# Kernel tuning notes

Measured on AMD Instinct MI355X. Metric: run time of the kernel, lower is better.

## Reference

```python
import jax, jax.numpy as jnp
import numpy as np
from jax import lax

BN_EPS = 1e-5
LRELU_SLOPE = 0.01  # nn.LeakyReLU default negative_slope


def setup_inputs() -> dict:
    key = jax.random.key(0)
    k1, k2, k3, k4 = jax.random.split(key, 4)
    N, Cin, Cout, K, P = 500000, 32, 32, 27, 250000
    features = jax.random.normal(k1, (N, Cin), dtype=jnp.float32)
    weight = jax.random.normal(k2, (K, Cin, Cout), dtype=jnp.float32) * 0.05
    gamma = jnp.ones((Cout,), dtype=jnp.float32)
    beta = jnp.zeros((Cout,), dtype=jnp.float32)
    pairs_in = jax.random.randint(k3, (K, P), 0, N, dtype=jnp.int32)
    pairs_out = jax.random.randint(k4, (K, P), 0, N, dtype=jnp.int32)
    return {"features": features, "weight": weight, "gamma": gamma,
            "beta": beta, "pairs_in": pairs_in, "pairs_out": pairs_out}


def _subm_conv(features, weight, pairs_in, pairs_out):
    # Submanifold sparse conv: for each kernel offset k, gather input rows,
    # multiply by W[k], scatter-add into output rows. N_out == N_in.
    N = features.shape[0]
    Cout = weight.shape[-1]
    out0 = jnp.zeros((N, Cout), dtype=features.dtype)

    def step(acc, xs):
        w_k, pi_k, po_k = xs                  # [Cin,Cout], [P], [P]
        gathered = features[pi_k]             # [P, Cin] gather
        contrib = gathered @ w_k              # [P, Cout]
        return acc.at[po_k].add(contrib), None  # scatter-add

    out, _ = lax.scan(step, out0, (weight, pairs_in, pairs_out))
    return out


def reference(features, weight, gamma, beta, pairs_in, pairs_out):
    conv = _subm_conv(features, weight, pairs_in, pairs_out)   # [N, Cout]
    # Original forward: features = norm(act(features)) -> LeakyReLU THEN BN
    act = jnp.where(conv >= 0, conv, LRELU_SLOPE * conv)
    mean = jnp.mean(act, axis=0)
    var = jnp.var(act, axis=0)                # BatchNorm1d training stats over N
    y = (act - mean) * lax.rsqrt(var + BN_EPS) * gamma + beta
    return y
```

## Files before the change

### kernel.cpp

```cpp
#include <hip/hip_runtime.h>
#include <hip/hip_fp16.h>

#define CIN 32
#define COUT 32
#define LRELU_SLOPE 0.01f
#define BN_EPS 1e-5f
#define CHUNK 2048
#define KMAX 27

typedef _Float16 half2_t __attribute__((ext_vector_type(2)));

#if __has_builtin(__builtin_amdgcn_fdot2)
#define FDOT2(a, b, c) __builtin_amdgcn_fdot2((a), (b), (c), false)
#else
static __device__ __forceinline__ float fdot2_sw(half2_t a, half2_t b, float c) {
    return (float)a.x * (float)b.x + (float)a.y * (float)b.y + c;
}
#define FDOT2(a, b, c) fdot2_sw((a), (b), (c))
#endif

#if __has_builtin(__builtin_amdgcn_cvt_pkrtz)
#define CVTPK(x, y) __builtin_bit_cast(half2_t, __builtin_amdgcn_cvt_pkrtz((x), (y)))
#else
static __device__ __forceinline__ half2_t cvtpk_sw(float x, float y) {
    half2_t r; r.x = (_Float16)x; r.y = (_Float16)y; return r;
}
#define CVTPK(x, y) cvtpk_sw((x), (y))
#endif

union HU { uint4 u; half2_t h[4]; };
union FU { uint4 u; float f[4]; };


__global__ void __launch_bounds__(256) hist_kernel(
    const int* __restrict__ po, int* __restrict__ cnt, int E)
{
    int i0 = (blockIdx.x * blockDim.x + threadIdx.x) * 4;
    if (i0 + 3 < E) {
        int4 v = *(const int4*)(po + i0);
        atomicAdd(&cnt[v.x], 1);
        atomicAdd(&cnt[v.y], 1);
        atomicAdd(&cnt[v.z], 1);
        atomicAdd(&cnt[v.w], 1);
    } else {
        for (int i = i0; i < E; ++i) atomicAdd(&cnt[po[i]], 1);
    }
}

__global__ void __launch_bounds__(256) blocksum_kernel(
    const int* __restrict__ cnt, int* __restrict__ bsum, int N)
{
    int base = blockIdx.x * CHUNK + threadIdx.x * 8;
    int s = 0;
#pragma unroll
    for (int j = 0; j < 8; ++j) { int i = base + j; if (i < N) s += cnt[i]; }
#pragma unroll
    for (int off = 1; off < 64; off <<= 1) s += __shfl_xor(s, off);
    __shared__ int wsum[4];
    if ((threadIdx.x & 63) == 0) wsum[threadIdx.x >> 6] = s;
    __syncthreads();
    if (threadIdx.x == 0) bsum[blockIdx.x] = wsum[0] + wsum[1] + wsum[2] + wsum[3];
}

__global__ void __launch_bounds__(256) scanblk_kernel(
    const int* __restrict__ bsum, int* __restrict__ boffs, int nb)
{
    __shared__ int ts[256];
    int tid = threadIdx.x;
    int v[4]; int s = 0;
#pragma unroll
    for (int j = 0; j < 4; ++j) {
        int i = tid * 4 + j;
        v[j] = (i < nb) ? bsum[i] : 0;
        s += v[j];
    }
    ts[tid] = s;
    __syncthreads();
    for (int off = 1; off < 256; off <<= 1) {
        int add = (tid >= off) ? ts[tid - off] : 0;
        __syncthreads();
        ts[tid] += add;
        __syncthreads();
    }
    int run = ts[tid] - s;
#pragma unroll
    for (int j = 0; j < 4; ++j) {
        int i = tid * 4 + j;
        if (i < nb) { boffs[i] = run; run += v[j]; }
    }
}

__global__ void __launch_bounds__(256) scatteroffs_kernel(
    int* __restrict__ cnt, int* __restrict__ cursors,
    const int* __restrict__ boffs, int N)
{
    int tid = threadIdx.x;
    int lane = tid & 63;
    int wv = tid >> 6;
    int base = blockIdx.x * CHUNK + tid * 8;
    int c[8]; int tsum = 0;
#pragma unroll
    for (int j = 0; j < 8; ++j) { int i = base + j; c[j] = (i < N) ? cnt[i] : 0; tsum += c[j]; }
    int x = tsum;
#pragma unroll
    for (int off = 1; off < 64; off <<= 1) {
        int y = __shfl_up(x, off);
        if (lane >= off) x += y;
    }
    __shared__ int wtot[4];
    if (lane == 63) wtot[wv] = x;
    __syncthreads();
    int woff = boffs[blockIdx.x];
    for (int w = 0; w < wv; ++w) woff += wtot[w];
    int off = woff + x - tsum;
#pragma unroll
    for (int j = 0; j < 8; ++j) {
        int i = base + j;
        if (i < N) { cnt[i] = off; cursors[i] = off; off += c[j]; }
    }
}

__global__ void __launch_bounds__(256) scatter_kernel(
    const int* __restrict__ pairs_out, const int* __restrict__ pairs_in,
    int* __restrict__ cursors, int* __restrict__ sorted, int P)
{
    int p0 = (blockIdx.x * blockDim.x + threadIdx.x) * 4;
    int k = blockIdx.y;
    const int* po = pairs_out + (size_t)k * P;
    const int* pi = pairs_in + (size_t)k * P;
    if (p0 + 3 < P) {
        int4 o4 = *(const int4*)(po + p0);
        int4 i4 = *(const int4*)(pi + p0);
        int s0 = atomicAdd(&cursors[o4.x], 1); sorted[s0] = (i4.x << 6) | k;
        int s1 = atomicAdd(&cursors[o4.y], 1); sorted[s1] = (i4.y << 6) | k;
        int s2 = atomicAdd(&cursors[o4.z], 1); sorted[s2] = (i4.z << 6) | k;
        int s3 = atomicAdd(&cursors[o4.w], 1); sorted[s3] = (i4.w << 6) | k;
    } else {
        for (int p = p0; p < P; ++p) {
            int slot = atomicAdd(&cursors[po[p]], 1);
            sorted[slot] = (pi[p] << 6) | k;
        }
    }
}


__global__ void __launch_bounds__(256) cvt_kernel(
    const float* __restrict__ f, __half* __restrict__ o, int n8)
{
    int i = blockIdx.x * 256 + threadIdx.x;
    if (i >= n8) return;
    const float4* s = (const float4*)f + (size_t)i * 2;
    float4 a = s[0], b = s[1];
    union { uint4 u; __half h[8]; } r;
    r.h[0] = __float2half(a.x); r.h[1] = __float2half(a.y);
    r.h[2] = __float2half(a.z); r.h[3] = __float2half(a.w);
    r.h[4] = __float2half(b.x); r.h[5] = __float2half(b.y);
    r.h[6] = __float2half(b.z); r.h[7] = __float2half(b.w);
    ((uint4*)o)[i] = r.u;
}


template<int PC>
__global__ void __launch_bounds__(512, 8) fused_wave_kernel(
    const float* __restrict__ features,
    const __half* __restrict__ feat16,
    const float* __restrict__ weight,
    const int* __restrict__ sorted,
    const int* __restrict__ offsets,
    float* __restrict__ out,
    float* __restrict__ gstats,
    int N, int E, int rowBase, int rowCount, int rpw, int KW)
{
    __shared__ __align__(16) __half wlds[KMAX * 512];
    __shared__ float sred[8][16];
    __shared__ float qred[8][16];

    const int co_base = ((blockIdx.x >> 3) & 1) << 4;
    const int rg = (blockIdx.x & 7) | ((blockIdx.x >> 4) << 3);

    for (int s = threadIdx.x; s < KW * 512; s += 512) {
        int co_l = s & 15, c = (s >> 4) & 31, k = s >> 9;
        wlds[k * 512 + co_l * 32 + c] =
            __float2half(weight[k * 1024 + c * 32 + co_base + co_l]);
    }
    __syncthreads();

    const int lane = threadIdx.x & 63;
    const int wv = threadIdx.x >> 6;
    const int j = lane & 3;
    const int co_l = lane >> 2;
    const int gw = rg * 8 + wv;
    const int wlane_off = lane << 4;
    const char* wbase = (const char*)wlds;
    const char* fbase = PC ? (const char*)feat16 : (const char*)features;

    float ssum = 0.f, qsum = 0.f;

    int i0 = rowBase + gw * rpw;
    int i1 = i0 + rpw;
    int rend = rowBase + rowCount; if (rend > N) rend = N;
    if (i1 > rend) i1 = rend;

#define LOADE(F0, F1, W0, IDX) do {                                               \
    int _ii = (IDX); _ii = _ii < 63 ? _ii : 63;                                   \
    int _pk = __builtin_amdgcn_readlane(pkl, _ii);                                \
    W0 = *(const uint4*)(wbase + ((_pk & 63) << 10) + wlane_off);                 \
    if (PC) {                                                                     \
        const char* _sb = fbase + (unsigned)(_pk & 0xFFFFFFC0);                   \
        F0 = *(const uint4*)(_sb + (j << 4));                                     \
    } else {                                                                      \
        const char* _sb = fbase + ((size_t)(unsigned)(_pk & 0xFFFFFFC0) << 1);    \
        F0 = *(const uint4*)(_sb + (j << 5));                                     \
        F1 = *(const uint4*)(_sb + (j << 5) + 16);                                \
    }                                                                             \
} while (0)

#define DOTS(F0, F1, W0) do {                                                     \
    HU _w; _w.u = W0;                                                             \
    half2_t _p0, _p1, _p2, _p3;                                                   \
    if (PC) {                                                                     \
        HU _f; _f.u = F0;                                                         \
        _p0 = _f.h[0]; _p1 = _f.h[1]; _p2 = _f.h[2]; _p3 = _f.h[3];               \
    } else {                                                                      \
        FU _a, _b; _a.u = F0; _b.u = F1;                                          \
        _p0 = CVTPK(_a.f[0], _a.f[1]); _p1 = CVTPK(_a.f[2], _a.f[3]);             \
        _p2 = CVTPK(_b.f[0], _b.f[1]); _p3 = CVTPK(_b.f[2], _b.f[3]);             \
    }                                                                             \
    acc0 = FDOT2(_p0, _w.h[0], acc0); acc1 = FDOT2(_p1, _w.h[1], acc1);           \
    acc0 = FDOT2(_p2, _w.h[2], acc0); acc1 = FDOT2(_p3, _w.h[3], acc1);           \
} while (0)

#define WINDOW() do {                                                             \
    uint4 fA0, fA1, wA0, fB0, fB1, wB0, fC0, fC1, wC0, fD0, fD1, wD0;             \
    LOADE(fA0, fA1, wA0, 0);                                                      \
    LOADE(fB0, fB1, wB0, 1);                                                      \
    LOADE(fC0, fC1, wC0, 2);                                                      \
    LOADE(fD0, fD1, wD0, 3);                                                      \
    for (int e = 0; e < m; e += 4) {                                              \
        DOTS(fA0, fA1, wA0); LOADE(fA0, fA1, wA0, e + 4);                         \
        if (e + 1 < m) { DOTS(fB0, fB1, wB0); LOADE(fB0, fB1, wB0, e + 5); }      \
        if (e + 2 < m) { DOTS(fC0, fC1, wC0); LOADE(fC0, fC1, wC0, e + 6); }      \
        if (e + 3 < m) { DOTS(fD0, fD1, wD0); LOADE(fD0, fD1, wD0, e + 7); }      \
    }                                                                             \
} while (0)

    if (i0 < rend) {
        int beg = offsets[i0];
        int pklA;
        {
            int end0 = (i0 == N - 1) ? E : offsets[i0 + 1];
            int m0 = end0 - beg; if (m0 > 64) m0 = 64;
            pklA = (lane < m0) ? sorted[beg + lane] : 0;
        }
        for (int r = i0; r < i1; ++r) {
            int end = (r == N - 1) ? E : offsets[r + 1];
            int pklB = 0;
            if (r + 1 < i1) {
                int endn = (r + 1 == N - 1) ? E : offsets[r + 2];
                int mn = endn - end; if (mn > 64) mn = 64;
                pklB = (lane < mn) ? sorted[end + lane] : 0;
            }
            float acc0 = 0.f, acc1 = 0.f;
            if (end > beg) {
                {
                    int m = end - beg; if (m > 64) m = 64;
                    int pkl = pklA;
                    WINDOW();
                }
                for (int base = beg + 64; base < end; base += 64) {
                    int m = end - base; if (m > 64) m = 64;
                    int pkl = (lane < m) ? sorted[base + lane] : 0;
                    WINDOW();
                }
            }
            float acc = acc0 + acc1;
            acc += __shfl_xor(acc, 1);
            acc += __shfl_xor(acc, 2);
            float act = acc >= 0.f ? acc : LRELU_SLOPE * acc;
            if (j == 0) out[(size_t)r * COUT + co_base + co_l] = act;
            ssum += act; qsum += act * act;
            beg = end; pklA = pklB;
        }
    }

#undef WINDOW
#undef LOADE
#undef DOTS

    sred[wv][co_l] = ssum;
    qred[wv][co_l] = qsum;
    __syncthreads();
    if (threadIdx.x < 16) {
        int t = threadIdx.x;
        float S = 0.f, Q = 0.f;
#pragma unroll
        for (int w = 0; w < 8; ++w) { S += sred[w][t]; Q += qred[w][t]; }
        atomicAdd(&gstats[co_base + t], S);
        atomicAdd(&gstats[32 + co_base + t], Q);
    }
}

__global__ void __launch_bounds__(256) norm2_kernel(
    float* __restrict__ data, const float* __restrict__ stats,
    const float* __restrict__ gamma, const float* __restrict__ beta,
    int n4, float invN)
{
    int i = blockIdx.x * blockDim.x + threadIdx.x;
    if (i >= n4) return;
    int qd = i & 7;
    float sc[4], bs[4];
#pragma unroll
    for (int j = 0; j < 4; ++j) {
        int c = qd * 4 + j;
        float m = stats[c] * invN;
        float v = stats[32 + c] * invN - m * m;
        float inv = rsqrtf(v + BN_EPS);
        sc[j] = inv * gamma[c];
        bs[j] = beta[c] - m * sc[j];
    }
    float4* d4 = (float4*)data;
    float4 a = d4[i];
    float4 y;
    y.x = a.x * sc[0] + bs[0];
    y.y = a.y * sc[1] + bs[1];
    y.z = a.z * sc[2] + bs[2];
    y.w = a.w * sc[3] + bs[3];
    d4[i] = y;
}


__global__ void __launch_bounds__(256) conv_atomic_kernel(
    const float* __restrict__ features,
    const float* __restrict__ weight,
    const int* __restrict__ pairs_in,
    const int* __restrict__ pairs_out,
    float* __restrict__ out,
    int P)
{
    int p = blockIdx.x * blockDim.x + threadIdx.x;
    int k = blockIdx.y;
    if (p >= P) return;
    int pi = pairs_in[(size_t)k * P + p];
    int po = pairs_out[(size_t)k * P + p];
    const float4* __restrict__ frow = (const float4*)(features + (size_t)pi * CIN);
    const float* __restrict__ wk = weight + (size_t)k * CIN * COUT;
    float acc[COUT];
#pragma unroll
    for (int co = 0; co < COUT; ++co) acc[co] = 0.f;
#pragma unroll
    for (int c4 = 0; c4 < CIN / 4; ++c4) {
        float4 f = frow[c4];
        float fv[4] = {f.x, f.y, f.z, f.w};
#pragma unroll
        for (int j = 0; j < 4; ++j) {
            const float* __restrict__ wr = wk + (c4 * 4 + j) * COUT;
#pragma unroll
            for (int co = 0; co < COUT; ++co)
                acc[co] = fmaf(fv[j], wr[co], acc[co]);
        }
    }
    float* orow = out + (size_t)po * COUT;
#pragma unroll
    for (int co = 0; co < COUT; ++co)
        atomicAdd(orow + co, acc[co]);
}

__device__ __forceinline__ float4 lrelu4(float4 v) {
    float4 a;
    a.x = v.x >= 0.f ? v.x : LRELU_SLOPE * v.x;
    a.y = v.y >= 0.f ? v.y : LRELU_SLOPE * v.y;
    a.z = v.z >= 0.f ? v.z : LRELU_SLOPE * v.z;
    a.w = v.w >= 0.f ? v.w : LRELU_SLOPE * v.w;
    return a;
}

__global__ void __launch_bounds__(256) stats_fb_kernel(
    const float* __restrict__ conv, float* __restrict__ stats, int n4)
{
    const float4* __restrict__ c4p = (const float4*)conv;
    int stride = blockDim.x * gridDim.x;
    float4 s = {0.f, 0.f, 0.f, 0.f};
    float4 q = {0.f, 0.f, 0.f, 0.f};
    for (int i = blockIdx.x * blockDim.x + threadIdx.x; i < n4; i += stride) {
        float4 a = lrelu4(c4p[i]);
        s.x += a.x; s.y += a.y; s.z += a.z; s.w += a.w;
        q.x += a.x * a.x; q.y += a.y * a.y; q.z += a.z * a.z; q.w += a.w * a.w;
    }
#pragma unroll
    for (int off = 8; off < 64; off <<= 1) {
        s.x += __shfl_xor(s.x, off); s.y += __shfl_xor(s.y, off);
        s.z += __shfl_xor(s.z, off); s.w += __shfl_xor(s.w, off);
        q.x += __shfl_xor(q.x, off); q.y += __shfl_xor(q.y, off);
        q.z += __shfl_xor(q.z, off); q.w += __shfl_xor(q.w, off);
    }
    __shared__ float4 rs[4][8];
    __shared__ float4 rq[4][8];
    int lane = threadIdx.x & 63;
    int w = threadIdx.x >> 6;
    if (lane < 8) { rs[w][lane] = s; rq[w][lane] = q; }
    __syncthreads();
    if (threadIdx.x < 8) {
        int qd = threadIdx.x;
        float4 S = {0.f, 0.f, 0.f, 0.f};
        float4 Q = {0.f, 0.f, 0.f, 0.f};
        for (int ww = 0; ww < 4; ++ww) {
            float4 a = rs[ww][qd], b = rq[ww][qd];
            S.x += a.x; S.y += a.y; S.z += a.z; S.w += a.w;
            Q.x += b.x; Q.y += b.y; Q.z += b.z; Q.w += b.w;
        }
        atomicAdd(&stats[qd * 4 + 0], S.x); atomicAdd(&stats[qd * 4 + 1], S.y);
        atomicAdd(&stats[qd * 4 + 2], S.z); atomicAdd(&stats[qd * 4 + 3], S.w);
        atomicAdd(&stats[32 + qd * 4 + 0], Q.x); atomicAdd(&stats[32 + qd * 4 + 1], Q.y);
        atomicAdd(&stats[32 + qd * 4 + 2], Q.z); atomicAdd(&stats[32 + qd * 4 + 3], Q.w);
    }
}

__global__ void __launch_bounds__(256) norm_fb_kernel(
    float* __restrict__ data, const float* __restrict__ stats,
    const float* __restrict__ gamma, const float* __restrict__ beta,
    int n4, float invN)
{
    int i = blockIdx.x * blockDim.x + threadIdx.x;
    if (i >= n4) return;
    int qd = i & 7;
    float sc[4], bs[4];
#pragma unroll
    for (int j = 0; j < 4; ++j) {
        int c = qd * 4 + j;
        float m = stats[c] * invN;
        float v = stats[32 + c] * invN - m * m;
        float inv = rsqrtf(v + BN_EPS);
        sc[j] = inv * gamma[c];
        bs[j] = beta[c] - m * sc[j];
    }
    float4* d4 = (float4*)data;
    float4 a = lrelu4(d4[i]);
    float4 y;
    y.x = a.x * sc[0] + bs[0];
    y.y = a.y * sc[1] + bs[1];
    y.z = a.z * sc[2] + bs[2];
    y.w = a.w * sc[3] + bs[3];
    d4[i] = y;
}

extern "C" void kernel_launch(void* const* d_in, const int* in_sizes, int n_in,
                              void* d_out, int out_size, void* d_ws, size_t ws_size,
                              hipStream_t stream) {
    const float* features = (const float*)d_in[0];
    const float* weight   = (const float*)d_in[1];
    const float* gamma    = (const float*)d_in[2];
    const float* beta     = (const float*)d_in[3];
    const int* pairs_in   = (const int*)d_in[4];
    const int* pairs_out  = (const int*)d_in[5];
    float* out = (float*)d_out;

    int N  = in_sizes[0] / CIN;
    int KW = in_sizes[1] / (CIN * COUT);
    int P  = in_sizes[4] / KW;
    int E  = KW * P;
    int n4 = N * (COUT / 4);

    char* wsb = (char*)d_ws;
    float* stats  = (float*)wsb;
    int* offsets  = (int*)(wsb + 256);
    int* cursors  = offsets + N;
    int* bsum     = cursors + N;
    int* boffs    = bsum + 1024;
    int* sorted   = boffs + 1024;
    __half* feat16 = (__half*)(((uintptr_t)(sorted + E) + 15) & ~(uintptr_t)15);

    size_t need1 = 256 + ((size_t)2 * N + 2048 + E) * 4;
    size_t need2 = need1 + 16 + (size_t)N * CIN * 2;

    bool fast = (ws_size >= need1) && (KW <= KMAX) && (N <= (1 << 24));
    bool preconv = fast && (ws_size >= need2);

    if (fast) {
        hipMemsetAsync(stats, 0, 256, stream);
        hipMemsetAsync(offsets, 0, (size_t)N * sizeof(int), stream);

        hist_kernel<<<(E / 4 + 255) / 256, 256, 0, stream>>>(pairs_out, offsets, E);

        int nb = (N + CHUNK - 1) / CHUNK;
        blocksum_kernel<<<nb, 256, 0, stream>>>(offsets, bsum, N);
        scanblk_kernel<<<1, 256, 0, stream>>>(bsum, boffs, nb);
        scatteroffs_kernel<<<nb, 256, 0, stream>>>(offsets, cursors, boffs, N);

        dim3 sgrid((P + 1023) / 1024, KW);
        scatter_kernel<<<sgrid, 256, 0, stream>>>(pairs_out, pairs_in, cursors, sorted, P);

        const int NRG = 512;
        int totW = NRG * 8;
        int rows0 = (N + 1) / 2;
        int rows1 = N - rows0;
        int rpw0 = (rows0 + totW - 1) / totW;
        int rpw1 = (rows1 + totW - 1) / totW;

        if (preconv) {
            cvt_kernel<<<(N * (CIN / 8) + 255) / 256, 256, 0, stream>>>(
                features, feat16, N * (CIN / 8));
            fused_wave_kernel<1><<<NRG * 2, 512, 0, stream>>>(
                features, feat16, weight, sorted, offsets, out, stats,
                N, E, 0, rows0, rpw0, KW);
            fused_wave_kernel<1><<<NRG * 2, 512, 0, stream>>>(
                features, feat16, weight, sorted, offsets, out, stats,
                N, E, rows0, rows1, rpw1, KW);
        } else {
            fused_wave_kernel<0><<<NRG * 2, 512, 0, stream>>>(
                features, feat16, weight, sorted, offsets, out, stats,
                N, E, 0, rows0, rpw0, KW);
            fused_wave_kernel<0><<<NRG * 2, 512, 0, stream>>>(
                features, feat16, weight, sorted, offsets, out, stats,
                N, E, rows0, rows1, rpw1, KW);
        }

        norm2_kernel<<<(n4 + 255) / 256, 256, 0, stream>>>(out, stats, gamma, beta,
                                                           n4, 1.0f / (float)N);
    } else {
        hipMemsetAsync(d_out, 0, (size_t)out_size * sizeof(float), stream);
        hipMemsetAsync(d_ws, 0, 64 * sizeof(float), stream);
        dim3 cgrid((P + 255) / 256, KW);
        conv_atomic_kernel<<<cgrid, 256, 0, stream>>>(features, weight, pairs_in,
                                                      pairs_out, (float*)d_out, P);
        stats_fb_kernel<<<512, 256, 0, stream>>>((const float*)d_out, (float*)d_ws, n4);
        norm_fb_kernel<<<(n4 + 255) / 256, 256, 0, stream>>>((float*)d_out, (float*)d_ws,
                                                             gamma, beta, n4,
                                                             1.0f / (float)N);
    }
}
```

Before: 1.442 ms.

## Sort pairs in two phases via coarse bucket binning before atomic scatter

Replaces the single random-scatter counting-sort pass with a two-phase approach: pairs are first binned into 256 coarse buckets of output rows using shared-memory local histograms and staging, then a resolve pass does the per-row atomic scatter. Because binned entries are grouped by output range, the per-row cursor atomics and sorted writes in the resolve pass become more localized and cache-friendly. In exchange it adds an extra E*8-byte intermediate buffer, an extra read/write pass over all pairs, and two more kernel launches. It only runs when the workspace is large enough.

```diff
diff --git a/kernel.cpp b/kernel.cpp
--- a/kernel.cpp
+++ b/kernel.cpp
@@ -7,6 +7,8 @@
 #define BN_EPS 1e-5f
 #define CHUNK 2048
 #define KMAX 27
+#define NBUCK 256
+#define BCH 4096
 
 typedef _Float16 half2_t __attribute__((ext_vector_type(2)));
 
@@ -117,6 +119,114 @@
     for (int j = 0; j < 8; ++j) {
         int i = base + j;
         if (i < N) { cnt[i] = off; cursors[i] = off; off += c[j]; }
+    }
+}
+
+
+__global__ void __launch_bounds__(256) bucketinit_kernel(
+    const int* __restrict__ offsets, int* __restrict__ bucketCur,
+    int N, int E, int shift)
+{
+    int b = threadIdx.x;
+    long idx = (long)b << shift;
+    bucketCur[b] = (idx < N) ? offsets[idx] : E;
+}
+
+__global__ void __launch_bounds__(256) bin_kernel(
+    const int* __restrict__ pairs_out, const int* __restrict__ pairs_in,
+    int* __restrict__ bucketCur, uint2* __restrict__ binned,
+    int P, int shift)
+{
+    __shared__ uint2 buf[BCH];
+    __shared__ int hist[NBUCK];
+    __shared__ int ts[NBUCK];
+    __shared__ int lbase[NBUCK];
+    __shared__ int gbase[NBUCK];
+    __shared__ int lcur[NBUCK];
+    int tid = threadIdx.x;
+    int k = blockIdx.y;
+    int p0 = blockIdx.x * BCH;
+    const int* po = pairs_out + (size_t)k * P;
+    const int* pi = pairs_in  + (size_t)k * P;
+
+    hist[tid] = 0;
+    __syncthreads();
+
+    int myP[16], myV[16];
+#pragma unroll
+    for (int j = 0; j < 4; ++j) {
+        int idx = p0 + j * 1024 + tid * 4;
+        if (idx + 3 < P) {
+            int4 o4 = *(const int4*)(po + idx);
+            int4 i4 = *(const int4*)(pi + idx);
+            myP[j*4+0] = o4.x; myV[j*4+0] = (i4.x << 6) | k;
+            myP[j*4+1] = o4.y; myV[j*4+1] = (i4.y << 6) | k;
+            myP[j*4+2] = o4.z; myV[j*4+2] = (i4.z << 6) | k;
+            myP[j*4+3] = o4.w; myV[j*4+3] = (i4.w << 6) | k;
+        } else {
+#pragma unroll
+            for (int q = 0; q < 4; ++q) {
+                int ii = idx + q;
+                if (ii < P) { myP[j*4+q] = po[ii]; myV[j*4+q] = (pi[ii] << 6) | k; }
+                else myP[j*4+q] = -1;
+            }
+        }
+    }
+#pragma unroll
+    for (int x = 0; x < 16; ++x)
+        if (myP[x] >= 0) atomicAdd(&hist[myP[x] >> shift], 1);
+    __syncthreads();
+
+    int h = hist[tid];
+    ts[tid] = h;
+    __syncthreads();
+    for (int off = 1; off < NBUCK; off <<= 1) {
+        int add = (tid >= off) ? ts[tid - off] : 0;
+        __syncthreads();
+        ts[tid] += add;
+        __syncthreads();
+    }
+    lbase[tid] = ts[tid] - h;
+    lcur[tid]  = ts[tid] - h;
+    if (h > 0) gbase[tid] = atomicAdd(&bucketCur[tid], h);
+    __syncthreads();
+
+#pragma unroll
+    for (int x = 0; x < 16; ++x) {
+        if (myP[x] >= 0) {
+            int b = myP[x] >> shift;
+            int pos = atomicAdd(&lcur[b], 1);
+            buf[pos] = make_uint2((unsigned)myP[x], (unsigned)myV[x]);
+        }
+    }
+    __syncthreads();
+    {
+        int n = hist[tid];
+        if (n > 0) {
+            int src = lbase[tid], dst = gbase[tid];
+            for (int i = 0; i < n; ++i) binned[dst + i] = buf[src + i];
+        }
+    }
+}
+
+__global__ void __launch_bounds__(256) resolve_kernel(
+    const uint2* __restrict__ binned, int* __restrict__ cursors,
+    int* __restrict__ sorted, int E)
+{
+    int i0 = (blockIdx.x * 256 + threadIdx.x) * 4;
+    if (i0 + 3 < E) {
+        uint4 a = *(const uint4*)(binned + i0);
+        uint4 b = *(const uint4*)(binned + i0 + 2);
+        int s0 = atomicAdd(&cursors[a.x], 1); sorted[s0] = (int)a.y;
+        int s1 = atomicAdd(&cursors[a.z], 1); sorted[s1] = (int)a.w;
+        int s2 = atomicAdd(&cursors[b.x], 1); sorted[s2] = (int)b.y;
+        int s3 = atomicAdd(&cursors[b.z], 1); sorted[s3] = (int)b.w;
+    } else {
+        for (int i = i0; i < E; ++i) {
+            uint2 e = binned[i];
+            int s = atomicAdd(&cursors[e.x], 1);
+            sorted[s] = (int)e.y;
+        }
     }
 }
 
@@ -468,12 +578,16 @@
     int* boffs    = bsum + 1024;
     int* sorted   = boffs + 1024;
     __half* feat16 = (__half*)(((uintptr_t)(sorted + E) + 15) & ~(uintptr_t)15);
+    int* bucketCur = (int*)(((uintptr_t)(feat16 + (size_t)N * CIN) + 15) & ~(uintptr_t)15);
+    uint2* binned  = (uint2*)(bucketCur + NBUCK);
 
     size_t need1 = 256 + ((size_t)2 * N + 2048 + E) * 4;
     size_t need2 = need1 + 16 + (size_t)N * CIN * 2;
+    size_t need3 = need2 + 16 + NBUCK * 4 + (size_t)E * 8;
 
     bool fast = (ws_size >= need1) && (KW <= KMAX) && (N <= (1 << 24));
     bool preconv = fast && (ws_size >= need2);
+    bool twophase = preconv && (ws_size >= need3);
 
     if (fast) {
         hipMemsetAsync(stats, 0, 256, stream);
@@ -486,8 +600,20 @@
         scanblk_kernel<<<1, 256, 0, stream>>>(bsum, boffs, nb);
         scatteroffs_kernel<<<nb, 256, 0, stream>>>(offsets, cursors, boffs, N);
 
-        dim3 sgrid((P + 1023) / 1024, KW);
-        scatter_kernel<<<sgrid, 256, 0, stream>>>(pairs_out, pairs_in, cursors, sorted, P);
+        if (twophase) {
+            int shift = 0;
+            while (((N - 1) >> shift) >= NBUCK) shift++;
+            bucketinit_kernel<<<1, NBUCK, 0, stream>>>(offsets, bucketCur, N, E, shift);
+            dim3 bgrid((P + BCH - 1) / BCH, KW);
+            bin_kernel<<<bgrid, 256, 0, stream>>>(pairs_out, pairs_in, bucketCur,
+                                                  binned, P, shift);
+            resolve_kernel<<<(E + 1023) / 1024, 256, 0, stream>>>(binned, cursors,
+                                                                  sorted, E);
+        } else {
+            dim3 sgrid((P + 1023) / 1024, KW);
+            scatter_kernel<<<sgrid, 256, 0, stream>>>(pairs_out, pairs_in, cursors,
+                                                      sorted, P);
+        }
 
         const int NRG = 512;
         int totW = NRG * 8;
```

Result: slower. 1.517 ms (+5.2%).
